# Kernel optimization log

Hardware: AMD Instinct MI355X
Metric: run time of the kernel (lower is better)

Reference implementation:

```python
import jax, jax.numpy as jnp
import numpy as np

B, T, F, U = 32, 2048, 512, 512


def hard_sigmoid(x):
    # Keras hard_sigmoid: clip(0.2*x + 0.5, 0, 1)
    return jnp.clip(0.2 * x + 0.5, 0.0, 1.0)


def setup_inputs() -> dict:
    key = jax.random.key(0)
    ks = jax.random.split(key, 10)
    s = 0.05  # keep pre-activations in a sane range
    return {
        "x": jax.random.normal(ks[0], (B, F), jnp.float32),
        "h": jax.random.normal(ks[1], (B, U), jnp.float32),
        "annotations": jax.random.normal(ks[2], (B, T, F), jnp.float32),
        "kernel": jax.random.normal(ks[3], (F, 3 * U), jnp.float32) * s,
        "recurrent_kernel": jax.random.normal(ks[4], (U, 3 * U), jnp.float32) * s,
        "attention_kernel": jax.random.normal(ks[5], (F, 3 * U), jnp.float32) * s,
        "Wa": jax.random.normal(ks[6], (U, U), jnp.float32) * s,
        "Ua": jax.random.normal(ks[7], (F, U), jnp.float32) * s,
        "Va": jax.random.normal(ks[8], (U,), jnp.float32) * s,
        "bias": jnp.zeros((3 * U,), jnp.float32),
        "attention_bias": jnp.zeros((3 * U,), jnp.float32),
        "Wa_bias": jnp.zeros((U,), jnp.float32),
        "Ua_bias": jnp.zeros((U,), jnp.float32),
    }


def reference(x, h, annotations, kernel, recurrent_kernel, attention_kernel,
              Wa, Ua, Va, bias, attention_bias, Wa_bias, Ua_bias):
    u = h.shape[-1]
    # --- Bahdanau additive attention ---
    # pre: [B, T, U] = Wa h_{t-1} (broadcast over T) + Ua a_j
    pre = (h @ Wa + Wa_bias)[:, None, :] + annotations @ Ua + Ua_bias
    scores = jnp.einsum('btu,u->bt', jnp.tanh(pre), Va)          # [B, T]
    alpha = jax.nn.softmax(scores, axis=-1)                      # [B, T]
    c = jnp.einsum('bt,btf->bf', alpha, annotations)             # context [B, F]

    # --- GRU gates (reset_after=False, implementation 1 math, batched) ---
    xm = x @ kernel + bias                                       # [B, 3U]
    am = c @ attention_kernel + attention_bias                   # [B, 3U]
    x_z, x_r, x_h = xm[:, :u], xm[:, u:2 * u], xm[:, 2 * u:]
    a_z, a_r, a_h = am[:, :u], am[:, u:2 * u], am[:, 2 * u:]
    h_z = h @ recurrent_kernel[:, :u]
    h_r = h @ recurrent_kernel[:, u:2 * u]

    z = hard_sigmoid(x_z + h_z + a_z)                            # update gate
    r = hard_sigmoid(x_r + h_r + a_r)                            # reset gate
    hh = jnp.tanh(x_h + (r * h) @ recurrent_kernel[:, 2 * u:] + a_h)
    h_new = z * h + (1.0 - z) * hh
    return h_new
```

## Files before the change

### kernel.cpp

```cpp
#include <hip/hip_runtime.h>
#include <hip/hip_bf16.h>
#include <math.h>

#define BB 32
#define TT 2048
#define FF 512
#define UU 512

typedef __attribute__((ext_vector_type(4))) float f32x4;
typedef __attribute__((ext_vector_type(4))) short bf16x4;
typedef __attribute__((ext_vector_type(8))) short bf16x8;

__device__ inline short f2bf(float f) {
  union { __hip_bfloat16 h; short s; } u;
  u.h = __float2bfloat16(f);
  return u.s;
}

__device__ inline float tanh_fast(float x) {
  float e = __expf(2.0f * x);
  return 1.0f - 2.0f * __builtin_amdgcn_rcpf(e + 1.0f);
}


__global__ __launch_bounds__(256) void k1_hw(
    const float* __restrict__ h, const float* __restrict__ Wa,
    const float* __restrict__ Wa_bias, const float* __restrict__ Ua_bias,
    float* __restrict__ hw) {
  int idx = blockIdx.x * blockDim.x + threadIdx.x;
  int b = idx >> 9;
  int u = idx & 511;
  float acc = Wa_bias[u] + Ua_bias[u];
  const float* hrow = h + b * UU;
  for (int f = 0; f < FF; ++f) acc += hrow[f] * Wa[f * UU + u];
  hw[idx] = acc;
}

__global__ __launch_bounds__(64) void k0_pack(
    const float* __restrict__ Ua, short* __restrict__ Up) {
  const int n16 = blockIdx.x;
  const int k32 = blockIdx.y;
  const int l = threadIdx.x;
  const int n = n16 * 16 + (l & 15);
  const int g = l >> 4;
  bf16x8 v;
#pragma unroll
  for (int i = 0; i < 8; ++i) {
    int k = k32 * 32 + (i < 4 ? g * 4 + i : 16 + g * 4 + (i - 4));
    v[i] = f2bf(Ua[k * UU + n]);
  }
  *reinterpret_cast<bf16x8*>(Up + ((size_t)(n16 * 16 + k32) * 64 + l) * 8) = v;
}

__global__ __launch_bounds__(512, 4) void k2_flash(
    const float* __restrict__ ann, const short* __restrict__ Up,
    const float* __restrict__ Va, const float* __restrict__ hw,
    float* __restrict__ mbuf, float* __restrict__ lbuf,
    float* __restrict__ cpart) {
  __shared__ short Af[32768];
  __shared__ float red[8][64];
  __shared__ float e_all[64];
  const int tile = blockIdx.x;
  const int b = blockIdx.y;
  const int t0 = tile * 64;
  const int tid = threadIdx.x;
  const int w = tid >> 6;
  const int l = tid & 63;
  const int lo = l & 15;
  const int g = l >> 4;

  const float* annb = ann + ((size_t)b * TT + t0) * FF;

  {
    const int mf_s = w >> 1;
    const int kb_s = (w & 1) * 8;
#pragma unroll
    for (int v = 0; v < 8; ++v) {
      const int k32 = kb_s + v;
      const float* src = annb + (size_t)(mf_s * 16 + lo) * FF + k32 * 32 + g * 4;
      f32x4 a0 = *reinterpret_cast<const f32x4*>(src);
      f32x4 a1 = *reinterpret_cast<const f32x4*>(src + 16);
      bf16x8 o;
      o[0] = f2bf(a0.x); o[1] = f2bf(a0.y); o[2] = f2bf(a0.z); o[3] = f2bf(a0.w);
      o[4] = f2bf(a1.x); o[5] = f2bf(a1.y); o[6] = f2bf(a1.z); o[7] = f2bf(a1.w);
      *reinterpret_cast<bf16x8*>(&Af[((mf_s * 16 + k32) * 64 + l) * 8]) = o;
    }
  }
  __syncthreads();

  f32x4 acc[4][4];
#pragma unroll
  for (int mf = 0; mf < 4; ++mf)
#pragma unroll
    for (int nf = 0; nf < 4; ++nf) acc[mf][nf] = (f32x4)0.f;

  const short* upw = Up + ((size_t)(w * 4) * 16) * 64 * 8;
  bf16x8 bA[4], bB[4];
#pragma unroll
  for (int nf = 0; nf < 4; ++nf)
    bA[nf] = *reinterpret_cast<const bf16x8*>(
        Up + ((size_t)((w * 4 + nf) * 16 + 0) * 64 + l) * 8);
  (void)upw;

#pragma unroll
  for (int kk = 0; kk < 8; ++kk) {
    const int k0 = 2 * kk;
#pragma unroll
    for (int nf = 0; nf < 4; ++nf)
      bB[nf] = *reinterpret_cast<const bf16x8*>(
          Up + ((size_t)((w * 4 + nf) * 16 + k0 + 1) * 64 + l) * 8);
#pragma unroll
    for (int mf = 0; mf < 4; ++mf) {
      bf16x8 af = *reinterpret_cast<const bf16x8*>(
          &Af[((mf * 16 + k0) * 64 + l) * 8]);
#pragma unroll
      for (int nf = 0; nf < 4; ++nf)
        acc[mf][nf] = __builtin_amdgcn_mfma_f32_16x16x32_bf16(
            af, bA[nf], acc[mf][nf], 0, 0, 0);
    }
    if (kk < 7) {
#pragma unroll
      for (int nf = 0; nf < 4; ++nf)
        bA[nf] = *reinterpret_cast<const bf16x8*>(
            Up + ((size_t)((w * 4 + nf) * 16 + k0 + 2) * 64 + l) * 8);
    }
#pragma unroll
    for (int mf = 0; mf < 4; ++mf) {
      bf16x8 af = *reinterpret_cast<const bf16x8*>(
          &Af[((mf * 16 + k0 + 1) * 64 + l) * 8]);
#pragma unroll
      for (int nf = 0; nf < 4; ++nf)
        acc[mf][nf] = __builtin_amdgcn_mfma_f32_16x16x32_bf16(
            af, bB[nf], acc[mf][nf], 0, 0, 0);
    }
  }

  const float* hwb = hw + b * UU;
  float part[4][4];
#pragma unroll
  for (int mf = 0; mf < 4; ++mf)
#pragma unroll
    for (int r = 0; r < 4; ++r) part[mf][r] = 0.f;
#pragma unroll
  for (int nf = 0; nf < 4; ++nf) {
    const int u = w * 64 + nf * 16 + lo;
    const float hv = hwb[u];
    const float vv = Va[u];
#pragma unroll
    for (int mf = 0; mf < 4; ++mf)
#pragma unroll
      for (int r = 0; r < 4; ++r)
        part[mf][r] += tanh_fast(acc[mf][nf][r] + hv) * vv;
  }
#pragma unroll
  for (int mf = 0; mf < 4; ++mf)
#pragma unroll
    for (int r = 0; r < 4; ++r) {
      float s = part[mf][r];
      s += __shfl_xor(s, 1);
      s += __shfl_xor(s, 2);
      s += __shfl_xor(s, 4);
      s += __shfl_xor(s, 8);
      part[mf][r] = s;
    }
  if (lo == 0) {
#pragma unroll
    for (int mf = 0; mf < 4; ++mf)
#pragma unroll
      for (int r = 0; r < 4; ++r)
        red[w][mf * 16 + g * 4 + r] = part[mf][r];
  }
  __syncthreads();

  if (tid < 64) {
    float s = red[0][tid] + red[1][tid] + red[2][tid] + red[3][tid] +
              red[4][tid] + red[5][tid] + red[6][tid] + red[7][tid];
    float m = s;
#pragma unroll
    for (int off = 1; off < 64; off <<= 1) m = fmaxf(m, __shfl_xor(m, off));
    float e = __expf(s - m);
    float ls = e;
#pragma unroll
    for (int off = 1; off < 64; off <<= 1) ls += __shfl_xor(ls, off);
    e_all[tid] = e;
    if (tid == 0) {
      mbuf[b * 32 + tile] = m;
      lbuf[b * 32 + tile] = ls;
    }
  }
  __syncthreads();

  {
    const int f = tid;
    const int kk2 = f >> 5;
    const int q = (f >> 2) & 3;
    const int ib = (f & 3) + 4 * ((f >> 4) & 1);
    float a = 0.f;
    for (int it = 0; it < 64; ++it) {
      const int t = (it + tid) & 63;
      const int idx = (((t >> 4) * 16 + kk2) * 64 + q * 16 + (t & 15)) * 8 + ib;
      unsigned short vv = *reinterpret_cast<const unsigned short*>(&Af[idx]);
      a += e_all[t] * __uint_as_float(((unsigned)vv) << 16);
    }
    cpart[(size_t)(b * 32 + tile) * 512 + f] = a;
  }
}

__global__ __launch_bounds__(256) void k6_combine(
    const float* __restrict__ mbuf, const float* __restrict__ lbuf,
    const float* __restrict__ cpart, float* __restrict__ c) {
  const int b = blockIdx.x;
  const int tid = threadIdx.x;
  __shared__ float sm[32], sl[32];
  if (tid < 32) {
    sm[tid] = mbuf[b * 32 + tid];
    sl[tid] = lbuf[b * 32 + tid];
  }
  __syncthreads();
  float M = -1e30f;
#pragma unroll
  for (int i = 0; i < 32; ++i) M = fmaxf(M, sm[i]);
  float D = 0.f;
#pragma unroll
  for (int i = 0; i < 32; ++i) D += __expf(sm[i] - M) * sl[i];
  const float inv = 1.f / D;
  const int f = tid * 2;
  float a0 = 0.f, a1 = 0.f;
  for (int i = 0; i < 32; ++i) {
    const float wi = __expf(sm[i] - M);
    const float2 v = *reinterpret_cast<const float2*>(
        &cpart[(size_t)(b * 32 + i) * 512 + f]);
    a0 += wi * v.x;
    a1 += wi * v.y;
  }
  c[b * FF + f]     = a0 * inv;
  c[b * FF + f + 1] = a1 * inv;
}

__global__ __launch_bounds__(512) void k5a_gates(
    const float* __restrict__ x, const float* __restrict__ cc,
    const float* __restrict__ h, const float* __restrict__ kern,
    const float* __restrict__ ak, const float* __restrict__ rk,
    float* __restrict__ G) {
  __shared__ float wsx[64][64], wsa[64][64], wsr[64][64];
  __shared__ float xs[32][64], cs[32][64], hs[32][64];
  const int n0 = blockIdx.x * 64;
  const int kg0 = blockIdx.y * 64;
  const bool has_r = (n0 < 1024);
  const int tid = threadIdx.x;
  const int n = tid & 63;
  const int b0 = (tid >> 6) * 4;
  const int wrow = tid >> 3, wcol = (tid & 7) * 8;
  const int orow = tid >> 4, ocol = (tid & 15) * 4;
  float acc[4] = {0.f, 0.f, 0.f, 0.f};

  {
    const size_t wb = (size_t)(kg0 + wrow) * 1536 + n0 + wcol;
    *reinterpret_cast<float4*>(&wsx[wrow][wcol])     = *reinterpret_cast<const float4*>(kern + wb);
    *reinterpret_cast<float4*>(&wsx[wrow][wcol + 4]) = *reinterpret_cast<const float4*>(kern + wb + 4);
    *reinterpret_cast<float4*>(&wsa[wrow][wcol])     = *reinterpret_cast<const float4*>(ak + wb);
    *reinterpret_cast<float4*>(&wsa[wrow][wcol + 4]) = *reinterpret_cast<const float4*>(ak + wb + 4);
    if (has_r) {
      *reinterpret_cast<float4*>(&wsr[wrow][wcol])     = *reinterpret_cast<const float4*>(rk + wb);
      *reinterpret_cast<float4*>(&wsr[wrow][wcol + 4]) = *reinterpret_cast<const float4*>(rk + wb + 4);
    }
    *reinterpret_cast<float4*>(&xs[orow][ocol]) =
        *reinterpret_cast<const float4*>(x + orow * FF + kg0 + ocol);
    *reinterpret_cast<float4*>(&cs[orow][ocol]) =
        *reinterpret_cast<const float4*>(cc + orow * FF + kg0 + ocol);
    *reinterpret_cast<float4*>(&hs[orow][ocol]) =
        *reinterpret_cast<const float4*>(h + orow * UU + kg0 + ocol);
  }
  __syncthreads();
  if (has_r) {
#pragma unroll 8
    for (int k = 0; k < 64; ++k) {
      const float wx = wsx[k][n], wa = wsa[k][n], wr = wsr[k][n];
#pragma unroll
      for (int j = 0; j < 4; ++j)
        acc[j] += xs[b0 + j][k] * wx + cs[b0 + j][k] * wa + hs[b0 + j][k] * wr;
    }
  } else {
#pragma unroll 8
    for (int k = 0; k < 64; ++k) {
      const float wx = wsx[k][n], wa = wsa[k][n];
#pragma unroll
      for (int j = 0; j < 4; ++j)
        acc[j] += xs[b0 + j][k] * wx + cs[b0 + j][k] * wa;
    }
  }
#pragma unroll
  for (int j = 0; j < 4; ++j)
    atomicAdd(&G[(size_t)(b0 + j) * 1536 + n0 + n], acc[j]);
}

__global__ __launch_bounds__(256) void k5b_zr(
    const float* __restrict__ G, const float* __restrict__ h,
    const float* __restrict__ bias, const float* __restrict__ abias,
    float* __restrict__ zs, float* __restrict__ rh) {
  int idx = blockIdx.x * blockDim.x + threadIdx.x;
  int b = idx >> 9;
  int u = idx & 511;
  float z = 0.2f * (G[(size_t)b * 1536 + u] + bias[u] + abias[u]) + 0.5f;
  z = fminf(fmaxf(z, 0.f), 1.f);
  float r = 0.2f * (G[(size_t)b * 1536 + 512 + u] + bias[512 + u] + abias[512 + u]) + 0.5f;
  r = fminf(fmaxf(r, 0.f), 1.f);
  zs[idx] = z;
  rh[idx] = r * h[idx];
}

__global__ __launch_bounds__(512) void k5c_q(
    const float* __restrict__ rh, const float* __restrict__ rk,
    float* __restrict__ qbuf) {
  __shared__ float wsr[64][64];
  __shared__ float rs[32][64];
  const int n0 = blockIdx.x * 64;
  const int kg0 = blockIdx.y * 64;
  const int tid = threadIdx.x;
  const int n = tid & 63;
  const int b0 = (tid >> 6) * 4;
  const int wrow = tid >> 3, wcol = (tid & 7) * 8;
  const int orow = tid >> 4, ocol = (tid & 15) * 4;
  float acc[4] = {0.f, 0.f, 0.f, 0.f};

  {
    const size_t wb = (size_t)(kg0 + wrow) * 1536 + 1024 + n0 + wcol;
    *reinterpret_cast<float4*>(&wsr[wrow][wcol])     = *reinterpret_cast<const float4*>(rk + wb);
    *reinterpret_cast<float4*>(&wsr[wrow][wcol + 4]) = *reinterpret_cast<const float4*>(rk + wb + 4);
    *reinterpret_cast<float4*>(&rs[orow][ocol]) =
        *reinterpret_cast<const float4*>(rh + orow * UU + kg0 + ocol);
  }
  __syncthreads();
#pragma unroll 8
  for (int k = 0; k < 64; ++k) {
    const float w = wsr[k][n];
#pragma unroll
    for (int j = 0; j < 4; ++j) acc[j] += rs[b0 + j][k] * w;
  }
#pragma unroll
  for (int j = 0; j < 4; ++j)
    atomicAdd(&qbuf[(b0 + j) * UU + n0 + n], acc[j]);
}

__global__ __launch_bounds__(256) void k5d_out(
    const float* __restrict__ G, const float* __restrict__ qbuf,
    const float* __restrict__ zs, const float* __restrict__ h,
    const float* __restrict__ bias, const float* __restrict__ abias,
    float* __restrict__ out) {
  int idx = blockIdx.x * blockDim.x + threadIdx.x;
  int b = idx >> 9;
  int u = idx & 511;
  float hh = tanhf(G[(size_t)b * 1536 + 1024 + u] + bias[1024 + u] +
                   abias[1024 + u] + qbuf[idx]);
  float z = zs[idx];
  out[idx] = z * h[idx] + (1.f - z) * hh;
}

extern "C" void kernel_launch(void* const* d_in, const int* in_sizes, int n_in,
                              void* d_out, int out_size, void* d_ws, size_t ws_size,
                              hipStream_t stream) {
  const float* x       = (const float*)d_in[0];
  const float* h       = (const float*)d_in[1];
  const float* ann     = (const float*)d_in[2];
  const float* kern    = (const float*)d_in[3];
  const float* rk      = (const float*)d_in[4];
  const float* ak      = (const float*)d_in[5];
  const float* Wa      = (const float*)d_in[6];
  const float* Ua      = (const float*)d_in[7];
  const float* Va      = (const float*)d_in[8];
  const float* bias    = (const float*)d_in[9];
  const float* abias   = (const float*)d_in[10];
  const float* Wa_bias = (const float*)d_in[11];
  const float* Ua_bias = (const float*)d_in[12];

  float* ws     = (float*)d_ws;
  float* hw     = ws;
  float* mbuf   = ws + 16384;
  float* lbuf   = ws + 17408;
  float* cpart  = ws + 18432;
  float* c      = ws + 542720;
  float* G      = ws + 559104;
  float* qbuf   = ws + 608256;
  float* zs     = ws + 624640;
  float* rh     = ws + 641024;
  short* Up     = (short*)(ws + 657408);

  hipMemsetAsync(G, 0, 65536 * sizeof(float), stream);

  dim3 g0(32, 16);
  k0_pack<<<g0, 64, 0, stream>>>(Ua, Up);

  k1_hw<<<64, 256, 0, stream>>>(h, Wa, Wa_bias, Ua_bias, hw);

  dim3 g2(TT / 64, BB);
  k2_flash<<<g2, 512, 0, stream>>>(ann, Up, Va, hw, mbuf, lbuf, cpart);

  k6_combine<<<BB, 256, 0, stream>>>(mbuf, lbuf, cpart, c);

  dim3 g5a(24, 8);
  k5a_gates<<<g5a, 512, 0, stream>>>(x, c, h, kern, ak, rk, G);

  k5b_zr<<<64, 256, 0, stream>>>(G, h, bias, abias, zs, rh);

  dim3 g5c(8, 8);
  k5c_q<<<g5c, 512, 0, stream>>>(rh, rk, qbuf);

  k5d_out<<<64, 256, 0, stream>>>(G, qbuf, zs, h, bias, abias, (float*)d_out);
}
```

Baseline: 109.3 us.

## Halve attention tile to 32 timesteps, raise occupancy, store partial contexts in bf16

The flash-attention kernel now handles 32 timesteps per block instead of 64. This halves shared memory and accumulator registers, doubles the grid, and raises the launch-bounds occupancy hint from 4 to 8. Per-tile partial context vectors are written as bf16 to cut combine traffic. The combine kernel precomputes the per-tile softmax weights once in shared memory. The cost is that each block re-reads the full Ua weight panel, so weight traffic doubles, and the partial sums lose some precision.

```diff
diff --git a/kernel.cpp b/kernel.cpp
--- a/kernel.cpp
+++ b/kernel.cpp
@@ -52,17 +52,17 @@
   *reinterpret_cast<bf16x8*>(Up + ((size_t)(n16 * 16 + k32) * 64 + l) * 8) = v;
 }
 
-__global__ __launch_bounds__(512, 4) void k2_flash(
+__global__ __launch_bounds__(512, 8) void k2_flash(
     const float* __restrict__ ann, const short* __restrict__ Up,
     const float* __restrict__ Va, const float* __restrict__ hw,
     float* __restrict__ mbuf, float* __restrict__ lbuf,
-    float* __restrict__ cpart) {
-  __shared__ short Af[32768];
-  __shared__ float red[8][64];
-  __shared__ float e_all[64];
+    short* __restrict__ cpart) {
+  __shared__ short Af[16384];
+  __shared__ float red[8][32];
+  __shared__ float e_all[32];
   const int tile = blockIdx.x;
   const int b = blockIdx.y;
-  const int t0 = tile * 64;
+  const int t0 = tile * 32;
   const int tid = threadIdx.x;
   const int w = tid >> 6;
   const int l = tid & 63;
@@ -71,36 +71,35 @@
 
   const float* annb = ann + ((size_t)b * TT + t0) * FF;
 
-  {
-    const int mf_s = w >> 1;
-    const int kb_s = (w & 1) * 8;
-#pragma unroll
-    for (int v = 0; v < 8; ++v) {
-      const int k32 = kb_s + v;
-      const float* src = annb + (size_t)(mf_s * 16 + lo) * FF + k32 * 32 + g * 4;
-      f32x4 a0 = *reinterpret_cast<const f32x4*>(src);
-      f32x4 a1 = *reinterpret_cast<const f32x4*>(src + 16);
-      bf16x8 o;
-      o[0] = f2bf(a0.x); o[1] = f2bf(a0.y); o[2] = f2bf(a0.z); o[3] = f2bf(a0.w);
-      o[4] = f2bf(a1.x); o[5] = f2bf(a1.y); o[6] = f2bf(a1.z); o[7] = f2bf(a1.w);
-      *reinterpret_cast<bf16x8*>(&Af[((mf_s * 16 + k32) * 64 + l) * 8]) = o;
-    }
-  }
-  __syncthreads();
-
-  f32x4 acc[4][4];
-#pragma unroll
-  for (int mf = 0; mf < 4; ++mf)
+#pragma unroll
+  for (int v = 0; v < 4; ++v) {
+    const int E = v * 512 + tid;
+    const int mf = E >> 10;
+    const int k32 = (E >> 6) & 15;
+    const int slot = E & 63;
+    const int row = mf * 16 + (slot & 15);
+    const int gq = slot >> 4;
+    const float* src = annb + (size_t)row * FF + k32 * 32 + gq * 4;
+    f32x4 a0 = *reinterpret_cast<const f32x4*>(src);
+    f32x4 a1 = *reinterpret_cast<const f32x4*>(src + 16);
+    bf16x8 o;
+    o[0] = f2bf(a0.x); o[1] = f2bf(a0.y); o[2] = f2bf(a0.z); o[3] = f2bf(a0.w);
+    o[4] = f2bf(a1.x); o[5] = f2bf(a1.y); o[6] = f2bf(a1.z); o[7] = f2bf(a1.w);
+    *reinterpret_cast<bf16x8*>(&Af[E * 8]) = o;
+  }
+  __syncthreads();
+
+  f32x4 acc[2][4];
+#pragma unroll
+  for (int mf = 0; mf < 2; ++mf)
 #pragma unroll
     for (int nf = 0; nf < 4; ++nf) acc[mf][nf] = (f32x4)0.f;
 
-  const short* upw = Up + ((size_t)(w * 4) * 16) * 64 * 8;
   bf16x8 bA[4], bB[4];
 #pragma unroll
   for (int nf = 0; nf < 4; ++nf)
     bA[nf] = *reinterpret_cast<const bf16x8*>(
         Up + ((size_t)((w * 4 + nf) * 16 + 0) * 64 + l) * 8);
-  (void)upw;
 
 #pragma unroll
   for (int kk = 0; kk < 8; ++kk) {
@@ -110,7 +109,7 @@
       bB[nf] = *reinterpret_cast<const bf16x8*>(
           Up + ((size_t)((w * 4 + nf) * 16 + k0 + 1) * 64 + l) * 8);
 #pragma unroll
-    for (int mf = 0; mf < 4; ++mf) {
+    for (int mf = 0; mf < 2; ++mf) {
       bf16x8 af = *reinterpret_cast<const bf16x8*>(
           &Af[((mf * 16 + k0) * 64 + l) * 8]);
 #pragma unroll
@@ -125,7 +124,7 @@
             Up + ((size_t)((w * 4 + nf) * 16 + k0 + 2) * 64 + l) * 8);
     }
 #pragma unroll
-    for (int mf = 0; mf < 4; ++mf) {
+    for (int mf = 0; mf < 2; ++mf) {
       bf16x8 af = *reinterpret_cast<const bf16x8*>(
           &Af[((mf * 16 + k0 + 1) * 64 + l) * 8]);
 #pragma unroll
@@ -136,9 +135,9 @@
   }
 
   const float* hwb = hw + b * UU;
-  float part[4][4];
-#pragma unroll
-  for (int mf = 0; mf < 4; ++mf)
+  float part[2][4];
+#pragma unroll
+  for (int mf = 0; mf < 2; ++mf)
 #pragma unroll
     for (int r = 0; r < 4; ++r) part[mf][r] = 0.f;
 #pragma unroll
@@ -147,13 +146,13 @@
     const float hv = hwb[u];
     const float vv = Va[u];
 #pragma unroll
-    for (int mf = 0; mf < 4; ++mf)
+    for (int mf = 0; mf < 2; ++mf)
 #pragma unroll
       for (int r = 0; r < 4; ++r)
         part[mf][r] += tanh_fast(acc[mf][nf][r] + hv) * vv;
   }
 #pragma unroll
-  for (int mf = 0; mf < 4; ++mf)
+  for (int mf = 0; mf < 2; ++mf)
 #pragma unroll
     for (int r = 0; r < 4; ++r) {
       float s = part[mf][r];
@@ -165,27 +164,27 @@
     }
   if (lo == 0) {
 #pragma unroll
-    for (int mf = 0; mf < 4; ++mf)
+    for (int mf = 0; mf < 2; ++mf)
 #pragma unroll
       for (int r = 0; r < 4; ++r)
         red[w][mf * 16 + g * 4 + r] = part[mf][r];
   }
   __syncthreads();
 
-  if (tid < 64) {
+  if (tid < 32) {
     float s = red[0][tid] + red[1][tid] + red[2][tid] + red[3][tid] +
               red[4][tid] + red[5][tid] + red[6][tid] + red[7][tid];
     float m = s;
 #pragma unroll
-    for (int off = 1; off < 64; off <<= 1) m = fmaxf(m, __shfl_xor(m, off));
+    for (int off = 1; off < 32; off <<= 1) m = fmaxf(m, __shfl_xor(m, off));
     float e = __expf(s - m);
     float ls = e;
 #pragma unroll
-    for (int off = 1; off < 64; off <<= 1) ls += __shfl_xor(ls, off);
+    for (int off = 1; off < 32; off <<= 1) ls += __shfl_xor(ls, off);
     e_all[tid] = e;
     if (tid == 0) {
-      mbuf[b * 32 + tile] = m;
-      lbuf[b * 32 + tile] = ls;
+      mbuf[b * 64 + tile] = m;
+      lbuf[b * 64 + tile] = ls;
     }
   }
   __syncthreads();
@@ -196,42 +195,44 @@
     const int q = (f >> 2) & 3;
     const int ib = (f & 3) + 4 * ((f >> 4) & 1);
     float a = 0.f;
-    for (int it = 0; it < 64; ++it) {
-      const int t = (it + tid) & 63;
+    for (int it = 0; it < 32; ++it) {
+      const int t = (it + tid) & 31;
       const int idx = (((t >> 4) * 16 + kk2) * 64 + q * 16 + (t & 15)) * 8 + ib;
       unsigned short vv = *reinterpret_cast<const unsigned short*>(&Af[idx]);
       a += e_all[t] * __uint_as_float(((unsigned)vv) << 16);
     }
-    cpart[(size_t)(b * 32 + tile) * 512 + f] = a;
+    cpart[(size_t)(b * 64 + tile) * 512 + f] = f2bf(a);
   }
 }
 
 __global__ __launch_bounds__(256) void k6_combine(
     const float* __restrict__ mbuf, const float* __restrict__ lbuf,
-    const float* __restrict__ cpart, float* __restrict__ c) {
+    const short* __restrict__ cpart, float* __restrict__ c) {
   const int b = blockIdx.x;
   const int tid = threadIdx.x;
-  __shared__ float sm[32], sl[32];
-  if (tid < 32) {
-    sm[tid] = mbuf[b * 32 + tid];
-    sl[tid] = lbuf[b * 32 + tid];
+  __shared__ float sm[64], sl[64], sw[64];
+  if (tid < 64) {
+    sm[tid] = mbuf[b * 64 + tid];
+    sl[tid] = lbuf[b * 64 + tid];
   }
   __syncthreads();
   float M = -1e30f;
 #pragma unroll
-  for (int i = 0; i < 32; ++i) M = fmaxf(M, sm[i]);
+  for (int i = 0; i < 64; ++i) M = fmaxf(M, sm[i]);
+  if (tid < 64) sw[tid] = __expf(sm[tid] - M);
+  __syncthreads();
   float D = 0.f;
 #pragma unroll
-  for (int i = 0; i < 32; ++i) D += __expf(sm[i] - M) * sl[i];
+  for (int i = 0; i < 64; ++i) D += sw[i] * sl[i];
   const float inv = 1.f / D;
   const int f = tid * 2;
   float a0 = 0.f, a1 = 0.f;
-  for (int i = 0; i < 32; ++i) {
-    const float wi = __expf(sm[i] - M);
-    const float2 v = *reinterpret_cast<const float2*>(
-        &cpart[(size_t)(b * 32 + i) * 512 + f]);
-    a0 += wi * v.x;
-    a1 += wi * v.y;
+  for (int i = 0; i < 64; ++i) {
+    const unsigned vv = *reinterpret_cast<const unsigned*>(
+        &cpart[(size_t)(b * 64 + i) * 512 + f]);
+    const float wi = sw[i];
+    a0 += wi * __uint_as_float(vv << 16);
+    a1 += wi * __uint_as_float(vv & 0xffff0000u);
   }
   c[b * FF + f]     = a0 * inv;
   c[b * FF + f + 1] = a1 * inv;
@@ -373,17 +374,17 @@
   const float* Wa_bias = (const float*)d_in[11];
   const float* Ua_bias = (const float*)d_in[12];
 
-  float* ws     = (float*)d_ws;
-  float* hw     = ws;
-  float* mbuf   = ws + 16384;
-  float* lbuf   = ws + 17408;
-  float* cpart  = ws + 18432;
-  float* c      = ws + 542720;
-  float* G      = ws + 559104;
-  float* qbuf   = ws + 608256;
-  float* zs     = ws + 624640;
-  float* rh     = ws + 641024;
-  short* Up     = (short*)(ws + 657408);
+  float* ws      = (float*)d_ws;
+  float* hw      = ws;
+  float* mbuf    = ws + 16384;
+  float* lbuf    = ws + 18432;
+  short* cpart_h = (short*)(ws + 20480);
+  float* c       = ws + 544768;
+  float* G       = ws + 561152;
+  float* qbuf    = ws + 610304;
+  float* zs      = ws + 626688;
+  float* rh      = ws + 643072;
+  short* Up      = (short*)(ws + 659456);
 
   hipMemsetAsync(G, 0, 65536 * sizeof(float), stream);
 
@@ -392,10 +393,10 @@
 
   k1_hw<<<64, 256, 0, stream>>>(h, Wa, Wa_bias, Ua_bias, hw);
 
-  dim3 g2(TT / 64, BB);
-  k2_flash<<<g2, 512, 0, stream>>>(ann, Up, Va, hw, mbuf, lbuf, cpart);
-
-  k6_combine<<<BB, 256, 0, stream>>>(mbuf, lbuf, cpart, c);
+  dim3 g2(TT / 32, BB);
+  k2_flash<<<g2, 512, 0, stream>>>(ann, Up, Va, hw, mbuf, lbuf, cpart_h);
+
+  k6_combine<<<BB, 256, 0, stream>>>(mbuf, lbuf, cpart_h, c);
 
   dim3 g5a(24, 8);
   k5a_gates<<<g5a, 512, 0, stream>>>(x, c, h, kern, ak, rk, G);
```

Result: slower. 118.4 us (+8.3%).

## Double k2_flash block to 1024 threads, splitting U columns and context over time halves

Applied to the files above, without the earlier changes.

The attention flash kernel now runs with 16 waves per block instead of 8. Each wave handles 32 U columns instead of 64, which halves the accumulator registers per wave. The annotation staging is redistributed so each thread does 4 contiguous chunks instead of 8. The context reduction splits the 64 timesteps across two thread halves and combines them through shared memory. This is meant to raise latency hiding and parallelism, at the cost of an extra barrier, a larger reduction and more shared memory per block.

```diff
diff --git a/kernel.cpp b/kernel.cpp
--- a/kernel.cpp
+++ b/kernel.cpp
@@ -52,14 +52,15 @@
   *reinterpret_cast<bf16x8*>(Up + ((size_t)(n16 * 16 + k32) * 64 + l) * 8) = v;
 }
 
-__global__ __launch_bounds__(512, 4) void k2_flash(
+__global__ __launch_bounds__(1024, 8) void k2_flash(
     const float* __restrict__ ann, const short* __restrict__ Up,
     const float* __restrict__ Va, const float* __restrict__ hw,
     float* __restrict__ mbuf, float* __restrict__ lbuf,
     float* __restrict__ cpart) {
   __shared__ short Af[32768];
-  __shared__ float red[8][64];
+  __shared__ float red[16][64];
   __shared__ float e_all[64];
+  __shared__ float ctx[2][512];
   const int tile = blockIdx.x;
   const int b = blockIdx.y;
   const int t0 = tile * 64;
@@ -71,65 +72,64 @@
 
   const float* annb = ann + ((size_t)b * TT + t0) * FF;
 
-  {
-    const int mf_s = w >> 1;
-    const int kb_s = (w & 1) * 8;
-#pragma unroll
-    for (int v = 0; v < 8; ++v) {
-      const int k32 = kb_s + v;
-      const float* src = annb + (size_t)(mf_s * 16 + lo) * FF + k32 * 32 + g * 4;
-      f32x4 a0 = *reinterpret_cast<const f32x4*>(src);
-      f32x4 a1 = *reinterpret_cast<const f32x4*>(src + 16);
-      bf16x8 o;
-      o[0] = f2bf(a0.x); o[1] = f2bf(a0.y); o[2] = f2bf(a0.z); o[3] = f2bf(a0.w);
-      o[4] = f2bf(a1.x); o[5] = f2bf(a1.y); o[6] = f2bf(a1.z); o[7] = f2bf(a1.w);
-      *reinterpret_cast<bf16x8*>(&Af[((mf_s * 16 + k32) * 64 + l) * 8]) = o;
-    }
-  }
-  __syncthreads();
-
-  f32x4 acc[4][4];
+  bf16x8 bA[2], bB[2];
+#pragma unroll
+  for (int nf = 0; nf < 2; ++nf)
+    bA[nf] = *reinterpret_cast<const bf16x8*>(
+        Up + ((size_t)((w * 2 + nf) * 16 + 0) * 64 + l) * 8);
+
+#pragma unroll
+  for (int v = 0; v < 4; ++v) {
+    const int E = v * 1024 + tid;
+    const int mf = E >> 10;
+    const int k32 = (E >> 6) & 15;
+    const int slot = E & 63;
+    const int row = mf * 16 + (slot & 15);
+    const int gq = slot >> 4;
+    const float* src = annb + (size_t)row * FF + k32 * 32 + gq * 4;
+    f32x4 a0 = *reinterpret_cast<const f32x4*>(src);
+    f32x4 a1 = *reinterpret_cast<const f32x4*>(src + 16);
+    bf16x8 o;
+    o[0] = f2bf(a0.x); o[1] = f2bf(a0.y); o[2] = f2bf(a0.z); o[3] = f2bf(a0.w);
+    o[4] = f2bf(a1.x); o[5] = f2bf(a1.y); o[6] = f2bf(a1.z); o[7] = f2bf(a1.w);
+    *reinterpret_cast<bf16x8*>(&Af[E * 8]) = o;
+  }
+  __syncthreads();
+
+  f32x4 acc[4][2];
 #pragma unroll
   for (int mf = 0; mf < 4; ++mf)
 #pragma unroll
-    for (int nf = 0; nf < 4; ++nf) acc[mf][nf] = (f32x4)0.f;
-
-  const short* upw = Up + ((size_t)(w * 4) * 16) * 64 * 8;
-  bf16x8 bA[4], bB[4];
-#pragma unroll
-  for (int nf = 0; nf < 4; ++nf)
-    bA[nf] = *reinterpret_cast<const bf16x8*>(
-        Up + ((size_t)((w * 4 + nf) * 16 + 0) * 64 + l) * 8);
-  (void)upw;
+    for (int nf = 0; nf < 2; ++nf) acc[mf][nf] = (f32x4)0.f;
 
 #pragma unroll
   for (int kk = 0; kk < 8; ++kk) {
     const int k0 = 2 * kk;
 #pragma unroll
-    for (int nf = 0; nf < 4; ++nf)
+    for (int nf = 0; nf < 2; ++nf)
       bB[nf] = *reinterpret_cast<const bf16x8*>(
-          Up + ((size_t)((w * 4 + nf) * 16 + k0 + 1) * 64 + l) * 8);
+          Up + ((size_t)((w * 2 + nf) * 16 + k0 + 1) * 64 + l) * 8);
 #pragma unroll
     for (int mf = 0; mf < 4; ++mf) {
       bf16x8 af = *reinterpret_cast<const bf16x8*>(
           &Af[((mf * 16 + k0) * 64 + l) * 8]);
 #pragma unroll
-      for (int nf = 0; nf < 4; ++nf)
+      for (int nf = 0; nf < 2; ++nf)
         acc[mf][nf] = __builtin_amdgcn_mfma_f32_16x16x32_bf16(
             af, bA[nf], acc[mf][nf], 0, 0, 0);
     }
     if (kk < 7) {
 #pragma unroll
-      for (int nf = 0; nf < 4; ++nf)
+      for (int nf = 0; nf < 2; ++nf)
         bA[nf] = *reinterpret_cast<const bf16x8*>(
-            Up + ((size_t)((w * 4 + nf) * 16 + k0 + 2) * 64 + l) * 8);
+            Up + ((size_t)((w * 2 + nf) * 16 + k0 + 2) * 64 + l) * 8);
     }
 #pragma unroll
     for (int mf = 0; mf < 4; ++mf) {
       bf16x8 af = *reinterpret_cast<const bf16x8*>(
           &Af[((mf * 16 + k0 + 1) * 64 + l) * 8]);
 #pragma unroll
-      for (int nf = 0; nf < 4; ++nf)
+      for (int nf = 0; nf < 2; ++nf)
         acc[mf][nf] = __builtin_amdgcn_mfma_f32_16x16x32_bf16(
             af, bB[nf], acc[mf][nf], 0, 0, 0);
     }
@@ -142,8 +142,8 @@
 #pragma unroll
     for (int r = 0; r < 4; ++r) part[mf][r] = 0.f;
 #pragma unroll
-  for (int nf = 0; nf < 4; ++nf) {
-    const int u = w * 64 + nf * 16 + lo;
+  for (int nf = 0; nf < 2; ++nf) {
+    const int u = w * 32 + nf * 16 + lo;
     const float hv = hwb[u];
     const float vv = Va[u];
 #pragma unroll
@@ -173,8 +173,9 @@
   __syncthreads();
 
   if (tid < 64) {
-    float s = red[0][tid] + red[1][tid] + red[2][tid] + red[3][tid] +
-              red[4][tid] + red[5][tid] + red[6][tid] + red[7][tid];
+    float s = 0.f;
+#pragma unroll
+    for (int ww = 0; ww < 16; ++ww) s += red[ww][tid];
     float m = s;
 #pragma unroll
     for (int off = 1; off < 64; off <<= 1) m = fmaxf(m, __shfl_xor(m, off));
@@ -191,19 +192,23 @@
   __syncthreads();
 
   {
-    const int f = tid;
+    const int f = tid & 511;
+    const int th = tid >> 9;
     const int kk2 = f >> 5;
     const int q = (f >> 2) & 3;
     const int ib = (f & 3) + 4 * ((f >> 4) & 1);
     float a = 0.f;
-    for (int it = 0; it < 64; ++it) {
-      const int t = (it + tid) & 63;
+    for (int it = 0; it < 32; ++it) {
+      const int t = th * 32 + ((it + tid) & 31);
       const int idx = (((t >> 4) * 16 + kk2) * 64 + q * 16 + (t & 15)) * 8 + ib;
       unsigned short vv = *reinterpret_cast<const unsigned short*>(&Af[idx]);
       a += e_all[t] * __uint_as_float(((unsigned)vv) << 16);
     }
-    cpart[(size_t)(b * 32 + tile) * 512 + f] = a;
-  }
+    ctx[th][f] = a;
+  }
+  __syncthreads();
+  if (tid < 512)
+    cpart[(size_t)(b * 32 + tile) * 512 + tid] = ctx[0][tid] + ctx[1][tid];
 }
 
 __global__ __launch_bounds__(256) void k6_combine(
@@ -393,7 +398,7 @@
   k1_hw<<<64, 256, 0, stream>>>(h, Wa, Wa_bias, Ua_bias, hw);
 
   dim3 g2(TT / 64, BB);
-  k2_flash<<<g2, 512, 0, stream>>>(ann, Up, Va, hw, mbuf, lbuf, cpart);
+  k2_flash<<<g2, 1024, 0, stream>>>(ann, Up, Va, hw, mbuf, lbuf, cpart);
 
   k6_combine<<<BB, 256, 0, stream>>>(mbuf, lbuf, cpart, c);
 
```

After: 110.1 us. About the same (+0.7%).

## Double flash attention tile to 128 timesteps and vectorize context accumulation

Applied to the files above, without the earlier changes.

The attention-score kernel now processes 128 timesteps per block instead of 64. Each B-fragment of the packed Ua is reused across 8 M-fragments, which halves global reloads of Up per annotation row and halves the number of partial softmax outputs to combine. The context reduction is rewritten to read bf16x8 vectors split across 8 time-slices and reduced through shared memory, and MFMA phases are wrapped in s_setprio. The cost is double the LDS per block (about 128KB plus a 16KB context buffer), lower occupancy (launch bound 2), a grid of only 512 blocks, and more accumulator registers.

```diff
diff --git a/kernel.cpp b/kernel.cpp
--- a/kernel.cpp
+++ b/kernel.cpp
@@ -15,6 +15,10 @@
   union { __hip_bfloat16 h; short s; } u;
   u.h = __float2bfloat16(f);
   return u.s;
+}
+
+__device__ inline float bf2f(unsigned short s) {
+  return __uint_as_float(((unsigned)s) << 16);
 }
 
 __device__ inline float tanh_fast(float x) {
@@ -52,17 +56,20 @@
   *reinterpret_cast<bf16x8*>(Up + ((size_t)(n16 * 16 + k32) * 64 + l) * 8) = v;
 }
 
-__global__ __launch_bounds__(512, 4) void k2_flash(
+__global__ __launch_bounds__(512, 2) void k2_flash(
     const float* __restrict__ ann, const short* __restrict__ Up,
     const float* __restrict__ Va, const float* __restrict__ hw,
     float* __restrict__ mbuf, float* __restrict__ lbuf,
     float* __restrict__ cpart) {
-  __shared__ short Af[32768];
-  __shared__ float red[8][64];
-  __shared__ float e_all[64];
+  __shared__ short Af[65536];
+  __shared__ float red[8][128];
+  __shared__ float e_all[128];
+  __shared__ float sred[128];
+  __shared__ float wtmp[4];
+  __shared__ float ctxp[8][512];
   const int tile = blockIdx.x;
   const int b = blockIdx.y;
-  const int t0 = tile * 64;
+  const int t0 = tile * 128;
   const int tid = threadIdx.x;
   const int w = tid >> 6;
   const int l = tid & 63;
@@ -71,74 +78,87 @@
 
   const float* annb = ann + ((size_t)b * TT + t0) * FF;
 
-  {
-    const int mf_s = w >> 1;
-    const int kb_s = (w & 1) * 8;
-#pragma unroll
-    for (int v = 0; v < 8; ++v) {
-      const int k32 = kb_s + v;
-      const float* src = annb + (size_t)(mf_s * 16 + lo) * FF + k32 * 32 + g * 4;
-      f32x4 a0 = *reinterpret_cast<const f32x4*>(src);
-      f32x4 a1 = *reinterpret_cast<const f32x4*>(src + 16);
-      bf16x8 o;
-      o[0] = f2bf(a0.x); o[1] = f2bf(a0.y); o[2] = f2bf(a0.z); o[3] = f2bf(a0.w);
-      o[4] = f2bf(a1.x); o[5] = f2bf(a1.y); o[6] = f2bf(a1.z); o[7] = f2bf(a1.w);
-      *reinterpret_cast<bf16x8*>(&Af[((mf_s * 16 + k32) * 64 + l) * 8]) = o;
-    }
-  }
-  __syncthreads();
-
-  f32x4 acc[4][4];
-#pragma unroll
-  for (int mf = 0; mf < 4; ++mf)
+#pragma unroll
+  for (int v = 0; v < 16; ++v) {
+    const int E = v * 512 + tid;
+    const int fb = E >> 6;
+    const int mfb = fb >> 4;
+    const int k32 = fb & 15;
+    const int row = mfb * 16 + lo;
+    const float* src = annb + (size_t)row * FF + k32 * 32 + g * 4;
+    f32x4 a0 = *reinterpret_cast<const f32x4*>(src);
+    f32x4 a1 = *reinterpret_cast<const f32x4*>(src + 16);
+    bf16x8 o;
+    o[0] = f2bf(a0.x); o[1] = f2bf(a0.y); o[2] = f2bf(a0.z); o[3] = f2bf(a0.w);
+    o[4] = f2bf(a1.x); o[5] = f2bf(a1.y); o[6] = f2bf(a1.z); o[7] = f2bf(a1.w);
+    *reinterpret_cast<bf16x8*>(&Af[E * 8]) = o;
+  }
+  __syncthreads();
+
+  f32x4 acc[8][4];
+#pragma unroll
+  for (int mf = 0; mf < 8; ++mf)
 #pragma unroll
     for (int nf = 0; nf < 4; ++nf) acc[mf][nf] = (f32x4)0.f;
 
-  const short* upw = Up + ((size_t)(w * 4) * 16) * 64 * 8;
-  bf16x8 bA[4], bB[4];
-#pragma unroll
-  for (int nf = 0; nf < 4; ++nf)
-    bA[nf] = *reinterpret_cast<const bf16x8*>(
-        Up + ((size_t)((w * 4 + nf) * 16 + 0) * 64 + l) * 8);
-  (void)upw;
+  const short* upb0 = Up + ((size_t)((w * 4 + 0) * 16) * 64 + l) * 8;
+  const short* upb1 = Up + ((size_t)((w * 4 + 1) * 16) * 64 + l) * 8;
+  const short* upb2 = Up + ((size_t)((w * 4 + 2) * 16) * 64 + l) * 8;
+  const short* upb3 = Up + ((size_t)((w * 4 + 3) * 16) * 64 + l) * 8;
+
+  bf16x8 pA[4], pB[4];
+  pA[0] = *reinterpret_cast<const bf16x8*>(upb0);
+  pA[1] = *reinterpret_cast<const bf16x8*>(upb1);
+  pA[2] = *reinterpret_cast<const bf16x8*>(upb2);
+  pA[3] = *reinterpret_cast<const bf16x8*>(upb3);
+  pB[0] = *reinterpret_cast<const bf16x8*>(upb0 + 512);
+  pB[1] = *reinterpret_cast<const bf16x8*>(upb1 + 512);
+  pB[2] = *reinterpret_cast<const bf16x8*>(upb2 + 512);
+  pB[3] = *reinterpret_cast<const bf16x8*>(upb3 + 512);
 
 #pragma unroll
   for (int kk = 0; kk < 8; ++kk) {
     const int k0 = 2 * kk;
-#pragma unroll
-    for (int nf = 0; nf < 4; ++nf)
-      bB[nf] = *reinterpret_cast<const bf16x8*>(
-          Up + ((size_t)((w * 4 + nf) * 16 + k0 + 1) * 64 + l) * 8);
-#pragma unroll
-    for (int mf = 0; mf < 4; ++mf) {
+    __builtin_amdgcn_s_setprio(1);
+#pragma unroll
+    for (int mf = 0; mf < 8; ++mf) {
       bf16x8 af = *reinterpret_cast<const bf16x8*>(
           &Af[((mf * 16 + k0) * 64 + l) * 8]);
 #pragma unroll
       for (int nf = 0; nf < 4; ++nf)
         acc[mf][nf] = __builtin_amdgcn_mfma_f32_16x16x32_bf16(
-            af, bA[nf], acc[mf][nf], 0, 0, 0);
-    }
+            af, pA[nf], acc[mf][nf], 0, 0, 0);
+    }
+    __builtin_amdgcn_s_setprio(0);
     if (kk < 7) {
-#pragma unroll
-      for (int nf = 0; nf < 4; ++nf)
-        bA[nf] = *reinterpret_cast<const bf16x8*>(
-            Up + ((size_t)((w * 4 + nf) * 16 + k0 + 2) * 64 + l) * 8);
-    }
-#pragma unroll
-    for (int mf = 0; mf < 4; ++mf) {
+      pA[0] = *reinterpret_cast<const bf16x8*>(upb0 + (k0 + 2) * 512);
+      pA[1] = *reinterpret_cast<const bf16x8*>(upb1 + (k0 + 2) * 512);
+      pA[2] = *reinterpret_cast<const bf16x8*>(upb2 + (k0 + 2) * 512);
+      pA[3] = *reinterpret_cast<const bf16x8*>(upb3 + (k0 + 2) * 512);
+    }
+    __builtin_amdgcn_s_setprio(1);
+#pragma unroll
+    for (int mf = 0; mf < 8; ++mf) {
       bf16x8 af = *reinterpret_cast<const bf16x8*>(
           &Af[((mf * 16 + k0 + 1) * 64 + l) * 8]);
 #pragma unroll
       for (int nf = 0; nf < 4; ++nf)
         acc[mf][nf] = __builtin_amdgcn_mfma_f32_16x16x32_bf16(
-            af, bB[nf], acc[mf][nf], 0, 0, 0);
+            af, pB[nf], acc[mf][nf], 0, 0, 0);
+    }
+    __builtin_amdgcn_s_setprio(0);
+    if (kk < 7) {
+      pB[0] = *reinterpret_cast<const bf16x8*>(upb0 + (k0 + 3) * 512);
+      pB[1] = *reinterpret_cast<const bf16x8*>(upb1 + (k0 + 3) * 512);
+      pB[2] = *reinterpret_cast<const bf16x8*>(upb2 + (k0 + 3) * 512);
+      pB[3] = *reinterpret_cast<const bf16x8*>(upb3 + (k0 + 3) * 512);
     }
   }
 
   const float* hwb = hw + b * UU;
-  float part[4][4];
-#pragma unroll
-  for (int mf = 0; mf < 4; ++mf)
+  float part[8][4];
+#pragma unroll
+  for (int mf = 0; mf < 8; ++mf)
 #pragma unroll
     for (int r = 0; r < 4; ++r) part[mf][r] = 0.f;
 #pragma unroll
@@ -147,13 +167,13 @@
     const float hv = hwb[u];
     const float vv = Va[u];
 #pragma unroll
-    for (int mf = 0; mf < 4; ++mf)
+    for (int mf = 0; mf < 8; ++mf)
 #pragma unroll
       for (int r = 0; r < 4; ++r)
         part[mf][r] += tanh_fast(acc[mf][nf][r] + hv) * vv;
   }
 #pragma unroll
-  for (int mf = 0; mf < 4; ++mf)
+  for (int mf = 0; mf < 8; ++mf)
 #pragma unroll
     for (int r = 0; r < 4; ++r) {
       float s = part[mf][r];
@@ -165,44 +185,68 @@
     }
   if (lo == 0) {
 #pragma unroll
-    for (int mf = 0; mf < 4; ++mf)
+    for (int mf = 0; mf < 8; ++mf)
 #pragma unroll
       for (int r = 0; r < 4; ++r)
         red[w][mf * 16 + g * 4 + r] = part[mf][r];
   }
   __syncthreads();
 
-  if (tid < 64) {
+  if (tid < 128) {
     float s = red[0][tid] + red[1][tid] + red[2][tid] + red[3][tid] +
               red[4][tid] + red[5][tid] + red[6][tid] + red[7][tid];
+    sred[tid] = s;
     float m = s;
 #pragma unroll
     for (int off = 1; off < 64; off <<= 1) m = fmaxf(m, __shfl_xor(m, off));
-    float e = __expf(s - m);
+    if ((tid & 63) == 0) wtmp[tid >> 6] = m;
+  }
+  __syncthreads();
+  if (tid < 128) {
+    float m = fmaxf(wtmp[0], wtmp[1]);
+    float e = __expf(sred[tid] - m);
+    e_all[tid] = e;
     float ls = e;
 #pragma unroll
     for (int off = 1; off < 64; off <<= 1) ls += __shfl_xor(ls, off);
-    e_all[tid] = e;
-    if (tid == 0) {
-      mbuf[b * 32 + tile] = m;
-      lbuf[b * 32 + tile] = ls;
-    }
-  }
-  __syncthreads();
+    if ((tid & 63) == 0) wtmp[2 + (tid >> 6)] = ls;
+    if (tid == 0) mbuf[b * 16 + tile] = m;
+  }
+  __syncthreads();
+  if (tid == 0) lbuf[b * 16 + tile] = wtmp[2] + wtmp[3];
 
   {
-    const int f = tid;
-    const int kk2 = f >> 5;
-    const int q = (f >> 2) & 3;
-    const int ib = (f & 3) + 4 * ((f >> 4) & 1);
-    float a = 0.f;
-    for (int it = 0; it < 64; ++it) {
-      const int t = (it + tid) & 63;
-      const int idx = (((t >> 4) * 16 + kk2) * 64 + q * 16 + (t & 15)) * 8 + ib;
-      unsigned short vv = *reinterpret_cast<const unsigned short*>(&Af[idx]);
-      a += e_all[t] * __uint_as_float(((unsigned)vv) << 16);
-    }
-    cpart[(size_t)(b * 32 + tile) * 512 + f] = a;
+    const int fo = tid & 63;
+    const int ts = tid >> 6;
+    const int kk2 = fo >> 2;
+    const int gg = fo & 3;
+    float a8[8];
+#pragma unroll
+    for (int j = 0; j < 8; ++j) a8[j] = 0.f;
+#pragma unroll
+    for (int it = 0; it < 16; ++it) {
+      const int tl = (it + fo) & 15;
+      const int t = ts * 16 + tl;
+      const int entry = (ts * 16 + kk2) * 64 + gg * 16 + tl;
+      bf16x8 v = *reinterpret_cast<const bf16x8*>(&Af[entry * 8]);
+      const float e = e_all[t];
+#pragma unroll
+      for (int j = 0; j < 8; ++j)
+        a8[j] += e * bf2f((unsigned short)v[j]);
+    }
+#pragma unroll
+    for (int j = 0; j < 8; ++j) ctxp[ts][fo * 8 + j] = a8[j];
+  }
+  __syncthreads();
+  {
+    float s = 0.f;
+#pragma unroll
+    for (int ts2 = 0; ts2 < 8; ++ts2) s += ctxp[ts2][tid];
+    const int fo2 = tid >> 3;
+    const int j2 = tid & 7;
+    const int f = (fo2 >> 2) * 32 +
+                  ((j2 < 4) ? (fo2 & 3) * 4 + j2 : 16 + (fo2 & 3) * 4 + (j2 - 4));
+    cpart[(size_t)(b * 16 + tile) * 512 + f] = s;
   }
 }
 
@@ -211,25 +255,26 @@
     const float* __restrict__ cpart, float* __restrict__ c) {
   const int b = blockIdx.x;
   const int tid = threadIdx.x;
-  __shared__ float sm[32], sl[32];
-  if (tid < 32) {
-    sm[tid] = mbuf[b * 32 + tid];
-    sl[tid] = lbuf[b * 32 + tid];
+  __shared__ float sm[16], sl[16];
+  if (tid < 16) {
+    sm[tid] = mbuf[b * 16 + tid];
+    sl[tid] = lbuf[b * 16 + tid];
   }
   __syncthreads();
   float M = -1e30f;
 #pragma unroll
-  for (int i = 0; i < 32; ++i) M = fmaxf(M, sm[i]);
+  for (int i = 0; i < 16; ++i) M = fmaxf(M, sm[i]);
   float D = 0.f;
 #pragma unroll
-  for (int i = 0; i < 32; ++i) D += __expf(sm[i] - M) * sl[i];
+  for (int i = 0; i < 16; ++i) D += __expf(sm[i] - M) * sl[i];
   const float inv = 1.f / D;
   const int f = tid * 2;
   float a0 = 0.f, a1 = 0.f;
-  for (int i = 0; i < 32; ++i) {
+#pragma unroll
+  for (int i = 0; i < 16; ++i) {
     const float wi = __expf(sm[i] - M);
     const float2 v = *reinterpret_cast<const float2*>(
-        &cpart[(size_t)(b * 32 + i) * 512 + f]);
+        &cpart[(size_t)(b * 16 + i) * 512 + f]);
     a0 += wi * v.x;
     a1 += wi * v.y;
   }
@@ -376,14 +421,14 @@
   float* ws     = (float*)d_ws;
   float* hw     = ws;
   float* mbuf   = ws + 16384;
-  float* lbuf   = ws + 17408;
-  float* cpart  = ws + 18432;
-  float* c      = ws + 542720;
-  float* G      = ws + 559104;
-  float* qbuf   = ws + 608256;
-  float* zs     = ws + 624640;
-  float* rh     = ws + 641024;
-  short* Up     = (short*)(ws + 657408);
+  float* lbuf   = ws + 16896;
+  float* cpart  = ws + 17408;
+  float* c      = ws + 279552;
+  float* G      = ws + 295936;
+  float* qbuf   = ws + 345088;
+  float* zs     = ws + 361472;
+  float* rh     = ws + 377856;
+  short* Up     = (short*)(ws + 394240);
 
   hipMemsetAsync(G, 0, 65536 * sizeof(float), stream);
 
@@ -392,7 +437,7 @@
 
   k1_hw<<<64, 256, 0, stream>>>(h, Wa, Wa_bias, Ua_bias, hw);
 
-  dim3 g2(TT / 64, BB);
+  dim3 g2(TT / 128, BB);
   k2_flash<<<g2, 512, 0, stream>>>(ann, Up, Va, hw, mbuf, lbuf, cpart);
 
   k6_combine<<<BB, 256, 0, stream>>>(mbuf, lbuf, cpart, c);
```

Result: faster. 104.4 us (-4.5%).
